# Optimization experiments

Measured on AMD Instinct MI355X. Metric: run time of the kernel, lower is better.

## Reference

```python
import jax, jax.numpy as jnp
import numpy as np

NB = 2        # trm_num_blocks
H = 4         # trm_num_heads
D = 128       # trm_hidden_dim
L = 512
B = 1
PAD = 0
NEG = jnp.float32(-2**32 + 1)


def _ln(x, g, b, eps=1e-8):
    m = x.mean(-1, keepdims=True)
    v = x.var(-1, keepdims=True)
    return (x - m) / jnp.sqrt(v + eps) * g + b


def setup_inputs() -> dict:
    key = jax.random.key(0)
    ks = jax.random.split(key, 16)
    s = 0.02
    inp = {
        "log_seqs": jax.random.randint(ks[0], (B, L), 0, 1000),
        "seqs": jax.random.normal(ks[1], (B, L, D), jnp.float32),
        "time_matrix_K": jax.random.normal(ks[2], (B, L, L, D), jnp.float32),
        # per-block stacked params [NB, ...]
        "Wq": jax.random.normal(ks[3], (NB, D, D), jnp.float32) * s,
        "bq": jnp.zeros((NB, D), jnp.float32),
        "Wk": jax.random.normal(ks[4], (NB, D, D), jnp.float32) * s,
        "bk": jnp.zeros((NB, D), jnp.float32),
        "Wv": jax.random.normal(ks[5], (NB, D, D), jnp.float32) * s,
        "bv": jnp.zeros((NB, D), jnp.float32),
        "Wt": jax.random.normal(ks[6], (NB, D, D), jnp.float32) * s,
        "bt": jnp.zeros((NB, D), jnp.float32),
        "Wtp": jax.random.normal(ks[7], (NB, D, 1), jnp.float32) * s,
        "btp": jnp.zeros((NB, 1), jnp.float32),
        "ln1_g": jnp.ones((NB, D), jnp.float32),
        "ln1_b": jnp.zeros((NB, D), jnp.float32),
        "ln2_g": jnp.ones((NB, D), jnp.float32),
        "ln2_b": jnp.zeros((NB, D), jnp.float32),
        "W1": jax.random.normal(ks[8], (NB, D, D), jnp.float32) * s,
        "b1": jnp.zeros((NB, D), jnp.float32),
        "W2": jax.random.normal(ks[9], (NB, D, D), jnp.float32) * s,
        "b2": jnp.zeros((NB, D), jnp.float32),
        "lnf_g": jnp.ones((D,), jnp.float32),
        "lnf_b": jnp.zeros((D,), jnp.float32),
    }
    return inp


def reference(log_seqs, seqs, time_matrix_K, Wq, bq, Wk, bk, Wv, bv, Wt, bt,
              Wtp, btp, ln1_g, ln1_b, ln2_g, ln2_b, W1, b1, W2, b2, lnf_g, lnf_b):
    hd = D // H
    pad = (log_seqs == PAD)                     # [B, L] True at padding
    keep = (~pad)[..., None].astype(seqs.dtype)  # [B, L, 1]
    seqs = seqs * keep
    causal = ~jnp.tril(jnp.ones((L, L), bool))  # True above diagonal (masked)
    # combined mask [1, B, L, L]: pad query rows OR non-causal entries
    mask = pad[None, :, :, None] | causal[None, None, :, :]

    attn_ws = []
    for i in range(NB):
        Q = _ln(seqs, ln1_g[i], ln1_b[i])
        q = Q @ Wq[i] + bq[i]
        k = seqs @ Wk[i] + bk[i]
        v = seqs @ Wv[i] + bv[i]
        # head-major layout [H, B, L, hd] (matches torch split+cat along dim 0)
        qh = q.reshape(B, L, H, hd).transpose(2, 0, 1, 3)
        kh = k.reshape(B, L, H, hd).transpose(2, 0, 1, 3)
        vh = v.reshape(B, L, H, hd).transpose(2, 0, 1, 3)
        scores = jnp.einsum('hbqd,hbkd->hbqk', qh, kh)  # [H, B, L, L]
        # time bias: sigmoid(proj(relu(W_t t))) in (0,1); log is negative
        tw = jax.nn.sigmoid(
            (jax.nn.relu(time_matrix_K @ Wt[i] + bt[i]) @ Wtp[i] + btp[i]).squeeze(-1)
        )                                             # [B, L, L]
        scores = (scores + jnp.log(tw)) / jnp.float32(hd) ** 0.5
        scores = jnp.where(mask, NEG, scores)
        w = jax.nn.softmax(scores, axis=-1)           # dropout is identity (eval)
        attn_ws.append(w.reshape(H * B, L, L))
        out = jnp.einsum('hbqk,hbkd->hbqd', w, vh).transpose(1, 2, 0, 3).reshape(B, L, D)
        seqs = Q + out
        x = _ln(seqs, ln2_g[i], ln2_b[i])
        y = jax.nn.relu(x @ W1[i] + b1[i]) @ W2[i] + b2[i]
        seqs = (x + y) * keep                         # FFN residual adds post-LN x
    log_feats = _ln(seqs, lnf_g, lnf_b)
    return (log_feats, tuple(attn_ws))
```

## Files before the change

### kernel.cpp

```cpp
#include <hip/hip_runtime.h>

#define L 512
#define D 128
#define H 4
#define HD 32

typedef __bf16 bf16x8 __attribute__((ext_vector_type(8)));
typedef float  f32x4  __attribute__((ext_vector_type(4)));

__device__ __forceinline__ float wave_sum(float v){
#pragma unroll
  for (int o = 32; o; o >>= 1) v += __shfl_xor(v, o);
  return v;
}
__device__ __forceinline__ float wave_max(float v){
#pragma unroll
  for (int o = 32; o; o >>= 1) v = fmaxf(v, __shfl_xor(v, o));
  return v;
}

__global__ void k_bfrag(const float* __restrict__ Wt, unsigned short* __restrict__ bf){
  int idx = blockIdx.x * 256 + threadIdx.x;
  int jj   = idx & 7;
  int lane = (idx >> 3) & 63;
  int k0   = (idx >> 9) & 3;
  int nt   = idx >> 11;
  int d    = k0 * 32 + (lane >> 4) * 8 + jj;
  int col  = (nt & 7) * 16 + (lane & 15);
  int blk  = nt >> 3;
  float v = Wt[blk * D * D + d * D + col];
  __bf16 h = (__bf16)v;
  unsigned short us;
  __builtin_memcpy(&us, &h, 2);
  bf[idx] = us;
}

__global__ __launch_bounds__(256, 2) void k_timebias(
    const float* __restrict__ T, const unsigned short* __restrict__ bfg,
    const float* __restrict__ bt, const float* __restrict__ wtp,
    const float* __restrict__ btp, float* __restrict__ logtw){
  __shared__ __align__(16) unsigned short bsh[32768];
  __shared__ float bts[256], wtps[256];
  int tid = threadIdx.x;
  {
    const uint4* g = (const uint4*)bfg;
    uint4* s = (uint4*)bsh;
#pragma unroll
    for (int i = 0; i < 16; ++i) s[tid + i * 256] = g[tid + i * 256];
    bts[tid]  = bt[tid];
    wtps[tid] = wtp[tid];
  }
  __syncthreads();

  int lane = tid & 63, w = tid >> 6;
  int quad = lane >> 4, m = lane & 15;
  const bf16x8* bls = (const bf16x8*)bsh;
  int wbase = blockIdx.x * 256 + w * 64;

  bf16x8 afr[4][4];
#pragma unroll
  for (int mt = 0; mt < 4; ++mt){
    const float* tp = T + (size_t)(wbase + mt * 16 + m) * D + quad * 8;
#pragma unroll
    for (int k0 = 0; k0 < 4; ++k0){
      float4 f0 = *(const float4*)(tp + k0 * 32);
      float4 f1 = *(const float4*)(tp + k0 * 32 + 4);
      bf16x8 a;
      a[0] = (__bf16)f0.x; a[1] = (__bf16)f0.y; a[2] = (__bf16)f0.z; a[3] = (__bf16)f0.w;
      a[4] = (__bf16)f1.x; a[5] = (__bf16)f1.y; a[6] = (__bf16)f1.z; a[7] = (__bf16)f1.w;
      afr[mt][k0] = a;
    }
  }

#pragma unroll
  for (int blk = 0; blk < 2; ++blk){
    f32x4 rs[4] = {{0,0,0,0},{0,0,0,0},{0,0,0,0},{0,0,0,0}};
#pragma unroll
    for (int ntl = 0; ntl < 8; ++ntl){
      int nt = blk * 8 + ntl;
      f32x4 acc[4] = {{0,0,0,0},{0,0,0,0},{0,0,0,0},{0,0,0,0}};
#pragma unroll
      for (int k0 = 0; k0 < 4; ++k0){
        bf16x8 b = bls[(nt * 4 + k0) * 64 + lane];
#pragma unroll
        for (int mt = 0; mt < 4; ++mt)
          acc[mt] = __builtin_amdgcn_mfma_f32_16x16x32_bf16(afr[mt][k0], b, acc[mt], 0, 0, 0);
      }
      float btv = bts[nt * 16 + m];
      float wtv = wtps[nt * 16 + m];
#pragma unroll
      for (int mt = 0; mt < 4; ++mt)
#pragma unroll
        for (int r = 0; r < 4; ++r)
          rs[mt][r] += fmaxf(acc[mt][r] + btv, 0.f) * wtv;
    }
#pragma unroll
    for (int mt = 0; mt < 4; ++mt)
#pragma unroll
      for (int r = 0; r < 4; ++r){
        float v = rs[mt][r];
        v += __shfl_xor(v, 1); v += __shfl_xor(v, 2);
        v += __shfl_xor(v, 4); v += __shfl_xor(v, 8);
        rs[mt][r] = v;
      }
    if (m == 0){
      float bp = btp[blk];
      float* out = logtw + blk * (L * L);
#pragma unroll
      for (int mt = 0; mt < 4; ++mt){
        float4 o;
        float s0 = rs[mt][0] + bp; o.x = -logf(1.f + expf(-s0));
        float s1 = rs[mt][1] + bp; o.y = -logf(1.f + expf(-s1));
        float s2 = rs[mt][2] + bp; o.z = -logf(1.f + expf(-s2));
        float s3 = rs[mt][3] + bp; o.w = -logf(1.f + expf(-s3));
        *(float4*)(out + wbase + mt * 16 + quad * 4) = o;
      }
    }
  }
}

__global__ __launch_bounds__(128) void k_qkv(
    const float* __restrict__ src, const int* __restrict__ ls, int domask,
    const float* __restrict__ g1, const float* __restrict__ b1,
    const float* __restrict__ Wq, const float* __restrict__ bq,
    const float* __restrict__ Wk, const float* __restrict__ bk,
    const float* __restrict__ Wv, const float* __restrict__ bv,
    float* __restrict__ Q, float* __restrict__ qo,
    float* __restrict__ kT, float* __restrict__ vo){
  __shared__ float xs[128], Qs[128], tmp[2];
  int row = blockIdx.x, c = threadIdx.x;
  float xv = src[row * D + c];
  if (domask && ls[row] == 0) xv = 0.f;
  float s = wave_sum(xv);
  if ((c & 63) == 0) tmp[c >> 6] = s;
  __syncthreads();
  float mean = (tmp[0] + tmp[1]) * (1.f / 128.f);
  __syncthreads();
  float dv = xv - mean;
  float s2 = wave_sum(dv * dv);
  if ((c & 63) == 0) tmp[c >> 6] = s2;
  __syncthreads();
  float var = fmaxf((tmp[0] + tmp[1]) * (1.f / 128.f), 0.f);
  float qn = dv * rsqrtf(var + 1e-8f) * g1[c] + b1[c];
  xs[c] = xv; Qs[c] = qn;
  Q[row * D + c] = qn;
  __syncthreads();
  float aq = 0.f, ak = 0.f, av = 0.f;
#pragma unroll 4
  for (int k = 0; k < 128; ++k){
    float xq = Qs[k], xk = xs[k];
    aq += xq * Wq[k * D + c];
    ak += xk * Wk[k * D + c];
    av += xk * Wv[k * D + c];
  }
  aq += bq[c]; ak += bk[c]; av += bv[c];
  qo[row * D + c] = aq;
  vo[row * D + c] = av;
  kT[(c >> 5) * (HD * L) + (c & 31) * L + row] = ak;
}

__global__ __launch_bounds__(256) void k_attn_ffn(
    const float* __restrict__ qb, const float* __restrict__ kT, const float* __restrict__ vb,
    const float* __restrict__ logtw, const int* __restrict__ ls,
    const float* __restrict__ Q,
    const float* __restrict__ g2, const float* __restrict__ b2,
    const float* __restrict__ W1, const float* __restrict__ b1f,
    const float* __restrict__ W2, const float* __restrict__ b2f,
    const float* __restrict__ lg, const float* __restrict__ lb,
    float* __restrict__ wout, float* __restrict__ xout,
    float* __restrict__ lf, int last){
  __shared__ float qsh[128];
  __shared__ float sc[4][512];
  __shared__ float xr[128];
  __shared__ float x2s[128];
  __shared__ float y1s[128];
  __shared__ float pstore[256];
  __shared__ float st[2];
  int qr = blockIdx.x;
  int tid = threadIdx.x;
  int lane = tid & 63, h = tid >> 6;

  if (tid < 128) qsh[tid] = qb[qr * D + tid];
  __syncthreads();

  const float* kh = kT + h * (HD * L);
  const float* ltw = logtw + qr * L;
  const float RS = 0.17677669529663687f;
  float s[8];
#pragma unroll
  for (int jj = 0; jj < 8; ++jj){
    int j = jj * 64 + lane;
    float d = 0.f;
#pragma unroll
    for (int dd = 0; dd < 32; ++dd) d += qsh[h * HD + dd] * kh[dd * L + j];
    s[jj] = (d + ltw[j]) * RS;
  }
  bool padq = (ls[qr] == 0);
  float wgt[8];
  if (padq){
#pragma unroll
    for (int jj = 0; jj < 8; ++jj) wgt[jj] = 1.f / 512.f;
  } else {
    float mx = -3e38f;
#pragma unroll
    for (int jj = 0; jj < 8; ++jj){ int j = jj * 64 + lane; if (j <= qr) mx = fmaxf(mx, s[jj]); }
    mx = wave_max(mx);
    float sum = 0.f;
#pragma unroll
    for (int jj = 0; jj < 8; ++jj){
      int j = jj * 64 + lane;
      float e = (j <= qr) ? expf(s[jj] - mx) : 0.f;
      wgt[jj] = e; sum += e;
    }
    sum = wave_sum(sum);
    float inv = 1.f / sum;
#pragma unroll
    for (int jj = 0; jj < 8; ++jj) wgt[jj] *= inv;
  }
  float* wrow = wout + h * (L * L) + qr * L;
#pragma unroll
  for (int jj = 0; jj < 8; ++jj){
    int j = jj * 64 + lane;
    sc[h][j] = wgt[jj];
    wrow[j] = wgt[jj];
  }
  __syncthreads();

  int g = lane >> 5, d2 = lane & 31;
  const float* vh = vb + h * HD + d2;
  const float* sch = sc[h];
  float acc = 0.f;
  for (int j = g * 256; j < g * 256 + 256; ++j) acc += sch[j] * vh[(size_t)j * D];
  acc += __shfl_xor(acc, 32);
  if (g == 0){
    int idx = qr * D + h * HD + d2;
    xr[h * HD + d2] = Q[idx] + acc;
  }
  __syncthreads();

  if (tid < 64){
    float a = xr[tid], b = xr[tid + 64];
    float s1 = wave_sum(a + b);
    float s2 = wave_sum(a * a + b * b);
    if (tid == 0){
      float mean = s1 * (1.f / 128.f);
      float var = fmaxf(s2 * (1.f / 128.f) - mean * mean, 0.f);
      st[0] = mean; st[1] = rsqrtf(var + 1e-8f);
    }
  }
  __syncthreads();
  int c = tid & 127, half = tid >> 7;
  if (half == 0) x2s[c] = (xr[c] - st[0]) * st[1] * g2[c] + b2[c];
  __syncthreads();

  float a1 = 0.f;
  {
    int k0 = half * 64;
#pragma unroll 8
    for (int k = 0; k < 64; ++k) a1 += x2s[k0 + k] * W1[(k0 + k) * D + c];
  }
  pstore[tid] = a1;
  __syncthreads();
  if (half == 0) y1s[c] = fmaxf(pstore[c] + pstore[c + 128] + b1f[c], 0.f);
  __syncthreads();

  float a2 = 0.f;
  {
    int k0 = half * 64;
#pragma unroll 8
    for (int k = 0; k < 64; ++k) a2 += y1s[k0 + k] * W2[(k0 + k) * D + c];
  }
  pstore[tid] = a2;
  __syncthreads();
  float kp = (ls[qr] != 0) ? 1.f : 0.f;
  if (half == 0){
    float xo = (x2s[c] + pstore[c] + pstore[c + 128] + b2f[c]) * kp;
    xr[c] = xo;
    if (!last) xout[qr * D + c] = xo;
  }
  __syncthreads();

  if (last){
    if (tid < 64){
      float a = xr[tid], b = xr[tid + 64];
      float s1 = wave_sum(a + b);
      float s2 = wave_sum(a * a + b * b);
      if (tid == 0){
        float mean = s1 * (1.f / 128.f);
        float var = fmaxf(s2 * (1.f / 128.f) - mean * mean, 0.f);
        st[0] = mean; st[1] = rsqrtf(var + 1e-8f);
      }
    }
    __syncthreads();
    if (half == 0) lf[qr * D + c] = (xr[c] - st[0]) * st[1] * lg[c] + lb[c];
  }
}

extern "C" void kernel_launch(void* const* d_in, const int* in_sizes, int n_in,
                              void* d_out, int out_size, void* d_ws, size_t ws_size,
                              hipStream_t stream){
  const int*   ls   = (const int*)d_in[0];
  const float* seqs = (const float*)d_in[1];
  const float* T    = (const float*)d_in[2];
  const float* Wq   = (const float*)d_in[3];
  const float* bq   = (const float*)d_in[4];
  const float* Wk   = (const float*)d_in[5];
  const float* bk   = (const float*)d_in[6];
  const float* Wv   = (const float*)d_in[7];
  const float* bv   = (const float*)d_in[8];
  const float* Wt   = (const float*)d_in[9];
  const float* bt   = (const float*)d_in[10];
  const float* Wtp  = (const float*)d_in[11];
  const float* btp  = (const float*)d_in[12];
  const float* g1   = (const float*)d_in[13];
  const float* b1   = (const float*)d_in[14];
  const float* g2   = (const float*)d_in[15];
  const float* b2   = (const float*)d_in[16];
  const float* W1   = (const float*)d_in[17];
  const float* b1f  = (const float*)d_in[18];
  const float* W2   = (const float*)d_in[19];
  const float* b2f  = (const float*)d_in[20];
  const float* lg   = (const float*)d_in[21];
  const float* lb   = (const float*)d_in[22];

  float* ws   = (float*)d_ws;
  float* x    = ws;
  float* Q    = x + 65536;
  float* qb   = Q + 65536;
  float* vb   = qb + 65536;
  float* kT   = vb + 65536;
  float* logtw= kT + 65536;
  unsigned short* bfg = (unsigned short*)(logtw + 2 * 262144);

  float* outF = (float*)d_out;
  float* lf = outF;
  float* w0 = outF + 65536;
  float* w1 = w0 + 1048576;

  k_bfrag   <<<128, 256, 0, stream>>>(Wt, bfg);
  k_timebias<<<1024, 256, 0, stream>>>(T, bfg, bt, Wtp, btp, logtw);

  for (int blk = 0; blk < 2; ++blk){
    int o = blk * D * D, ob = blk * D;
    const float* src = blk ? x : seqs;
    k_qkv <<<512, 128, 0, stream>>>(src, ls, blk == 0 ? 1 : 0,
                                    g1 + ob, b1 + ob, Wq + o, bq + ob,
                                    Wk + o, bk + ob, Wv + o, bv + ob,
                                    Q, qb, kT, vb);
    k_attn_ffn<<<512, 256, 0, stream>>>(qb, kT, vb, logtw + blk * (L * L), ls,
                                        Q, g2 + ob, b2 + ob, W1 + o, b1f + ob,
                                        W2 + o, b2f + ob, lg, lb,
                                        blk ? w1 : w0, x, lf, blk);
  }
}
```

Baseline: 327.3 us.

## Use bf16 MFMA for attention and fuse next block's QKV into FFN kernel

Attention is rewritten to handle a 16-query tile per head per workgroup. QK^T and PV run on bf16 MFMA instructions, with Q, K and V stored in pre-swizzled bf16 fragment layouts and the softmax reduced across waves through shared memory. The FFN is split into its own kernel, and that kernel also computes LN1 plus the QKV projection for the next block, or the final LayerNorm. The aim is to replace scalar fp32 dot products with matrix-core work and to cut a launch and round trips. The cost is bf16 rounding of Q, K, V and the probabilities, which may affect accuracy, plus more launches for the attention/FFN split.

```diff
diff --git a/kernel.cpp b/kernel.cpp
--- a/kernel.cpp
+++ b/kernel.cpp
@@ -13,10 +13,11 @@
   for (int o = 32; o; o >>= 1) v += __shfl_xor(v, o);
   return v;
 }
-__device__ __forceinline__ float wave_max(float v){
-#pragma unroll
-  for (int o = 32; o; o >>= 1) v = fmaxf(v, __shfl_xor(v, o));
-  return v;
+__device__ __forceinline__ unsigned short bfbits(float v){
+  __bf16 h = (__bf16)v;
+  unsigned short u;
+  __builtin_memcpy(&u, &h, 2);
+  return u;
 }
 
 __global__ void k_bfrag(const float* __restrict__ Wt, unsigned short* __restrict__ bf){
@@ -28,11 +29,7 @@
   int d    = k0 * 32 + (lane >> 4) * 8 + jj;
   int col  = (nt & 7) * 16 + (lane & 15);
   int blk  = nt >> 3;
-  float v = Wt[blk * D * D + d * D + col];
-  __bf16 h = (__bf16)v;
-  unsigned short us;
-  __builtin_memcpy(&us, &h, 2);
-  bf[idx] = us;
+  bf[idx] = bfbits(Wt[blk * D * D + d * D + col]);
 }
 
 __global__ __launch_bounds__(256, 2) void k_timebias(
@@ -119,18 +116,35 @@
   }
 }
 
-__global__ __launch_bounds__(128) void k_qkv(
-    const float* __restrict__ src, const int* __restrict__ ls, int domask,
+__device__ __forceinline__ void write_qA(unsigned short* qA, int row, int c, float v){
+  int qt = row >> 4, m = row & 15;
+  int h = c >> 5, cc = c & 31;
+  qA[(((qt * 4 + h) * 64) + (cc >> 3) * 16 + m) * 8 + (cc & 7)] = bfbits(v);
+}
+__device__ __forceinline__ void write_kB(unsigned short* kB, int row, int c, float v){
+  int h = c >> 5, cc = c & 31;
+  int nt = row >> 4;
+  kB[((h * 32 + nt) * 64 + (cc >> 3) * 16 + (row & 15)) * 8 + (cc & 7)] = bfbits(v);
+}
+__device__ __forceinline__ void write_vB(unsigned short* vB, int row, int c, float v){
+  int h = c >> 5, cc = c & 31;
+  int kk = row >> 5, qv = (row >> 3) & 3, jv = row & 7;
+  int nt = cc >> 4;
+  vB[(((h * 16 + kk) * 2 + nt) * 64 + qv * 16 + (cc & 15)) * 8 + jv] = bfbits(v);
+}
+
+__global__ __launch_bounds__(128) void k_qkv0(
+    const float* __restrict__ src, const int* __restrict__ ls,
     const float* __restrict__ g1, const float* __restrict__ b1,
     const float* __restrict__ Wq, const float* __restrict__ bq,
     const float* __restrict__ Wk, const float* __restrict__ bk,
     const float* __restrict__ Wv, const float* __restrict__ bv,
-    float* __restrict__ Q, float* __restrict__ qo,
-    float* __restrict__ kT, float* __restrict__ vo){
+    float* __restrict__ Q, unsigned short* __restrict__ qA,
+    unsigned short* __restrict__ kB, unsigned short* __restrict__ vB){
   __shared__ float xs[128], Qs[128], tmp[2];
   int row = blockIdx.x, c = threadIdx.x;
   float xv = src[row * D + c];
-  if (domask && ls[row] == 0) xv = 0.f;
+  if (ls[row] == 0) xv = 0.f;
   float s = wave_sum(xv);
   if ((c & 63) == 0) tmp[c >> 6] = s;
   __syncthreads();
@@ -153,93 +167,157 @@
     ak += xk * Wk[k * D + c];
     av += xk * Wv[k * D + c];
   }
-  aq += bq[c]; ak += bk[c]; av += bv[c];
-  qo[row * D + c] = aq;
-  vo[row * D + c] = av;
-  kT[(c >> 5) * (HD * L) + (c & 31) * L + row] = ak;
-}
-
-__global__ __launch_bounds__(256) void k_attn_ffn(
-    const float* __restrict__ qb, const float* __restrict__ kT, const float* __restrict__ vb,
-    const float* __restrict__ logtw, const int* __restrict__ ls,
-    const float* __restrict__ Q,
+  write_qA(qA, row, c, aq + bq[c]);
+  write_kB(kB, row, c, ak + bk[c]);
+  write_vB(vB, row, c, av + bv[c]);
+}
+
+__global__ __launch_bounds__(256) void k_attn(
+    const unsigned short* __restrict__ qA, const unsigned short* __restrict__ kB,
+    const unsigned short* __restrict__ vB, const float* __restrict__ logtw,
+    const int* __restrict__ ls, const float* __restrict__ Q,
+    float* __restrict__ wout, float* __restrict__ xr){
+  __shared__ __align__(16) unsigned short pa[16 * 64 * 8];
+  __shared__ float pvp[4][2][64][4];
+  __shared__ float smax[4][16], ssum[4][16];
+  int qt = blockIdx.x >> 2, h = blockIdx.x & 3;
+  int tid = threadIdx.x, lane = tid & 63, w = tid >> 6;
+  int quad = lane >> 4, mcol = lane & 15;
+  const float RS = 0.17677669529663687f;
+
+  bf16x8 qf = ((const bf16x8*)qA)[(qt * 4 + h) * 64 + lane];
+
+  f32x4 acc[8];
+#pragma unroll
+  for (int nt8 = 0; nt8 < 8; ++nt8){
+    bf16x8 bf = ((const bf16x8*)kB)[(h * 32 + w * 8 + nt8) * 64 + lane];
+    f32x4 z = {0, 0, 0, 0};
+    acc[nt8] = __builtin_amdgcn_mfma_f32_16x16x32_bf16(qf, bf, z, 0, 0, 0);
+  }
+
+  float e[8][4];
+  float mx4[4] = {-3e38f, -3e38f, -3e38f, -3e38f};
+#pragma unroll
+  for (int nt8 = 0; nt8 < 8; ++nt8){
+    int col = w * 128 + nt8 * 16 + mcol;
+#pragma unroll
+    for (int r = 0; r < 4; ++r){
+      int row = qt * 16 + quad * 4 + r;
+      float sv = (acc[nt8][r] + logtw[row * L + col]) * RS;
+      sv = (col <= row) ? sv : -3e38f;
+      e[nt8][r] = sv;
+      mx4[r] = fmaxf(mx4[r], sv);
+    }
+  }
+#pragma unroll
+  for (int r = 0; r < 4; ++r){
+    float v = mx4[r];
+    v = fmaxf(v, __shfl_xor(v, 1)); v = fmaxf(v, __shfl_xor(v, 2));
+    v = fmaxf(v, __shfl_xor(v, 4)); v = fmaxf(v, __shfl_xor(v, 8));
+    mx4[r] = v;
+  }
+  if (mcol == 0){
+#pragma unroll
+    for (int r = 0; r < 4; ++r) smax[w][quad * 4 + r] = mx4[r];
+  }
+  __syncthreads();
+  float mxr[4], sum4[4] = {0, 0, 0, 0};
+#pragma unroll
+  for (int r = 0; r < 4; ++r){
+    int rr = quad * 4 + r;
+    mxr[r] = fmaxf(fmaxf(smax[0][rr], smax[1][rr]), fmaxf(smax[2][rr], smax[3][rr]));
+  }
+#pragma unroll
+  for (int nt8 = 0; nt8 < 8; ++nt8)
+#pragma unroll
+    for (int r = 0; r < 4; ++r){
+      float sv = e[nt8][r];
+      float ev = (sv > -1e38f) ? expf(sv - mxr[r]) : 0.f;
+      e[nt8][r] = ev;
+      sum4[r] += ev;
+    }
+#pragma unroll
+  for (int r = 0; r < 4; ++r){
+    float v = sum4[r];
+    v += __shfl_xor(v, 1); v += __shfl_xor(v, 2);
+    v += __shfl_xor(v, 4); v += __shfl_xor(v, 8);
+    sum4[r] = v;
+  }
+  if (mcol == 0){
+#pragma unroll
+    for (int r = 0; r < 4; ++r) ssum[w][quad * 4 + r] = sum4[r];
+  }
+  __syncthreads();
+  float inv[4]; int padr[4];
+#pragma unroll
+  for (int r = 0; r < 4; ++r){
+    int rr = quad * 4 + r;
+    inv[r] = 1.f / (ssum[0][rr] + ssum[1][rr] + ssum[2][rr] + ssum[3][rr]);
+    padr[r] = (ls[qt * 16 + rr] == 0);
+  }
+#pragma unroll
+  for (int nt8 = 0; nt8 < 8; ++nt8){
+    int col = w * 128 + nt8 * 16 + mcol;
+    int kk = col >> 5, qk = (col >> 3) & 3, jj = col & 7;
+#pragma unroll
+    for (int r = 0; r < 4; ++r){
+      int rl = quad * 4 + r;
+      float wv = padr[r] ? (1.f / 512.f) : e[nt8][r] * inv[r];
+      wout[h * (L * L) + (qt * 16 + rl) * L + col] = wv;
+      pa[(kk * 64 + qk * 16 + rl) * 8 + jj] = bfbits(wv);
+    }
+  }
+
+  f32x4 pacc[2] = {{0,0,0,0},{0,0,0,0}};
+#pragma unroll
+  for (int kk4 = 0; kk4 < 4; ++kk4){
+    int kk = w * 4 + kk4;
+    bf16x8 af = ((const bf16x8*)pa)[kk * 64 + lane];
+#pragma unroll
+    for (int nt = 0; nt < 2; ++nt){
+      bf16x8 bf = ((const bf16x8*)vB)[((h * 16 + kk) * 2 + nt) * 64 + lane];
+      pacc[nt] = __builtin_amdgcn_mfma_f32_16x16x32_bf16(af, bf, pacc[nt], 0, 0, 0);
+    }
+  }
+#pragma unroll
+  for (int nt = 0; nt < 2; ++nt)
+#pragma unroll
+    for (int r = 0; r < 4; ++r) pvp[w][nt][lane][r] = pacc[nt][r];
+  __syncthreads();
+  if (w < 2){
+    int nt = w;
+#pragma unroll
+    for (int r = 0; r < 4; ++r){
+      float o = pvp[0][nt][lane][r] + pvp[1][nt][lane][r]
+              + pvp[2][nt][lane][r] + pvp[3][nt][lane][r];
+      int row = qt * 16 + quad * 4 + r;
+      int cg = h * HD + nt * 16 + mcol;
+      xr[row * D + cg] = Q[row * D + cg] + o;
+    }
+  }
+}
+
+__global__ __launch_bounds__(256) void k_ffn(
+    const float* __restrict__ xr, const int* __restrict__ ls,
     const float* __restrict__ g2, const float* __restrict__ b2,
     const float* __restrict__ W1, const float* __restrict__ b1f,
     const float* __restrict__ W2, const float* __restrict__ b2f,
-    const float* __restrict__ lg, const float* __restrict__ lb,
-    float* __restrict__ wout, float* __restrict__ xout,
-    float* __restrict__ lf, int last){
-  __shared__ float qsh[128];
-  __shared__ float sc[4][512];
-  __shared__ float xr[128];
-  __shared__ float x2s[128];
-  __shared__ float y1s[128];
-  __shared__ float pstore[256];
-  __shared__ float st[2];
-  int qr = blockIdx.x;
-  int tid = threadIdx.x;
-  int lane = tid & 63, h = tid >> 6;
-
-  if (tid < 128) qsh[tid] = qb[qr * D + tid];
-  __syncthreads();
-
-  const float* kh = kT + h * (HD * L);
-  const float* ltw = logtw + qr * L;
-  const float RS = 0.17677669529663687f;
-  float s[8];
-#pragma unroll
-  for (int jj = 0; jj < 8; ++jj){
-    int j = jj * 64 + lane;
-    float d = 0.f;
-#pragma unroll
-    for (int dd = 0; dd < 32; ++dd) d += qsh[h * HD + dd] * kh[dd * L + j];
-    s[jj] = (d + ltw[j]) * RS;
-  }
-  bool padq = (ls[qr] == 0);
-  float wgt[8];
-  if (padq){
-#pragma unroll
-    for (int jj = 0; jj < 8; ++jj) wgt[jj] = 1.f / 512.f;
-  } else {
-    float mx = -3e38f;
-#pragma unroll
-    for (int jj = 0; jj < 8; ++jj){ int j = jj * 64 + lane; if (j <= qr) mx = fmaxf(mx, s[jj]); }
-    mx = wave_max(mx);
-    float sum = 0.f;
-#pragma unroll
-    for (int jj = 0; jj < 8; ++jj){
-      int j = jj * 64 + lane;
-      float e = (j <= qr) ? expf(s[jj] - mx) : 0.f;
-      wgt[jj] = e; sum += e;
-    }
-    sum = wave_sum(sum);
-    float inv = 1.f / sum;
-#pragma unroll
-    for (int jj = 0; jj < 8; ++jj) wgt[jj] *= inv;
-  }
-  float* wrow = wout + h * (L * L) + qr * L;
-#pragma unroll
-  for (int jj = 0; jj < 8; ++jj){
-    int j = jj * 64 + lane;
-    sc[h][j] = wgt[jj];
-    wrow[j] = wgt[jj];
-  }
-  __syncthreads();
-
-  int g = lane >> 5, d2 = lane & 31;
-  const float* vh = vb + h * HD + d2;
-  const float* sch = sc[h];
-  float acc = 0.f;
-  for (int j = g * 256; j < g * 256 + 256; ++j) acc += sch[j] * vh[(size_t)j * D];
-  acc += __shfl_xor(acc, 32);
-  if (g == 0){
-    int idx = qr * D + h * HD + d2;
-    xr[h * HD + d2] = Q[idx] + acc;
-  }
-  __syncthreads();
-
+    int fuse_qkv,
+    const float* __restrict__ g1, const float* __restrict__ b1,
+    const float* __restrict__ Wq, const float* __restrict__ bq,
+    const float* __restrict__ Wk, const float* __restrict__ bk,
+    const float* __restrict__ Wv, const float* __restrict__ bv,
+    float* __restrict__ Q, unsigned short* __restrict__ qA,
+    unsigned short* __restrict__ kB, unsigned short* __restrict__ vB,
+    int fuse_lnf, const float* __restrict__ lg, const float* __restrict__ lb,
+    float* __restrict__ lf){
+  __shared__ float xrs[128], x2s[128], y1s[128], pstore[256], st[2];
+  int row = blockIdx.x, tid = threadIdx.x;
+  int c = tid & 127, half = tid >> 7;
+  if (half == 0) xrs[c] = xr[row * D + c];
+  __syncthreads();
   if (tid < 64){
-    float a = xr[tid], b = xr[tid + 64];
+    float a = xrs[tid], b = xrs[tid + 64];
     float s1 = wave_sum(a + b);
     float s2 = wave_sum(a * a + b * b);
     if (tid == 0){
@@ -249,40 +327,30 @@
     }
   }
   __syncthreads();
-  int c = tid & 127, half = tid >> 7;
-  if (half == 0) x2s[c] = (xr[c] - st[0]) * st[1] * g2[c] + b2[c];
-  __syncthreads();
-
+  if (half == 0) x2s[c] = (xrs[c] - st[0]) * st[1] * g2[c] + b2[c];
+  __syncthreads();
   float a1 = 0.f;
-  {
-    int k0 = half * 64;
+  { int k0 = half * 64;
 #pragma unroll 8
-    for (int k = 0; k < 64; ++k) a1 += x2s[k0 + k] * W1[(k0 + k) * D + c];
-  }
+    for (int k = 0; k < 64; ++k) a1 += x2s[k0 + k] * W1[(k0 + k) * D + c]; }
   pstore[tid] = a1;
   __syncthreads();
   if (half == 0) y1s[c] = fmaxf(pstore[c] + pstore[c + 128] + b1f[c], 0.f);
   __syncthreads();
-
   float a2 = 0.f;
-  {
-    int k0 = half * 64;
+  { int k0 = half * 64;
 #pragma unroll 8
-    for (int k = 0; k < 64; ++k) a2 += y1s[k0 + k] * W2[(k0 + k) * D + c];
-  }
+    for (int k = 0; k < 64; ++k) a2 += y1s[k0 + k] * W2[(k0 + k) * D + c]; }
   pstore[tid] = a2;
   __syncthreads();
-  float kp = (ls[qr] != 0) ? 1.f : 0.f;
-  if (half == 0){
-    float xo = (x2s[c] + pstore[c] + pstore[c + 128] + b2f[c]) * kp;
-    xr[c] = xo;
-    if (!last) xout[qr * D + c] = xo;
-  }
-  __syncthreads();
-
-  if (last){
+  float kp = (ls[row] != 0) ? 1.f : 0.f;
+  if (half == 0)
+    xrs[c] = (x2s[c] + pstore[c] + pstore[c + 128] + b2f[c]) * kp;
+  __syncthreads();
+
+  if (fuse_qkv){
     if (tid < 64){
-      float a = xr[tid], b = xr[tid + 64];
+      float a = xrs[tid], b = xrs[tid + 64];
       float s1 = wave_sum(a + b);
       float s2 = wave_sum(a * a + b * b);
       if (tid == 0){
@@ -292,7 +360,47 @@
       }
     }
     __syncthreads();
-    if (half == 0) lf[qr * D + c] = (xr[c] - st[0]) * st[1] * lg[c] + lb[c];
+    if (half == 0){
+      float qn = (xrs[c] - st[0]) * st[1] * g1[c] + b1[c];
+      y1s[c] = qn;
+      Q[row * D + c] = qn;
+    }
+    __syncthreads();
+    float avp = 0.f;
+    if (half == 0){
+      float aq = 0.f;
+#pragma unroll 4
+      for (int k = 0; k < 128; ++k) aq += y1s[k] * Wq[k * D + c];
+#pragma unroll 8
+      for (int k = 0; k < 64; ++k) avp += xrs[k] * Wv[k * D + c];
+      write_qA(qA, row, c, aq + bq[c]);
+    } else {
+      float ak = 0.f;
+#pragma unroll 4
+      for (int k = 0; k < 128; ++k) ak += xrs[k] * Wk[k * D + c];
+#pragma unroll 8
+      for (int k = 64; k < 128; ++k) avp += xrs[k] * Wv[k * D + c];
+      write_kB(kB, row, c, ak + bk[c]);
+    }
+    pstore[tid] = avp;
+    __syncthreads();
+    if (half == 1)
+      write_vB(vB, row, c, pstore[c] + pstore[c + 128] + bv[c]);
+  }
+
+  if (fuse_lnf){
+    if (tid < 64){
+      float a = xrs[tid], b = xrs[tid + 64];
+      float s1 = wave_sum(a + b);
+      float s2 = wave_sum(a * a + b * b);
+      if (tid == 0){
+        float mean = s1 * (1.f / 128.f);
+        float var = fmaxf(s2 * (1.f / 128.f) - mean * mean, 0.f);
+        st[0] = mean; st[1] = rsqrtf(var + 1e-8f);
+      }
+    }
+    __syncthreads();
+    if (half == 0) lf[row * D + c] = (xrs[c] - st[0]) * st[1] * lg[c] + lb[c];
   }
 }
 
@@ -323,14 +431,14 @@
   const float* lg   = (const float*)d_in[21];
   const float* lb   = (const float*)d_in[22];
 
-  float* ws   = (float*)d_ws;
-  float* x    = ws;
-  float* Q    = x + 65536;
-  float* qb   = Q + 65536;
-  float* vb   = qb + 65536;
-  float* kT   = vb + 65536;
-  float* logtw= kT + 65536;
+  float* ws    = (float*)d_ws;
+  float* Q     = ws;
+  float* xr    = Q + 65536;
+  float* logtw = xr + 65536;
   unsigned short* bfg = (unsigned short*)(logtw + 2 * 262144);
+  unsigned short* qA  = bfg + 32768;
+  unsigned short* kB  = qA + 65536;
+  unsigned short* vB  = kB + 65536;
 
   float* outF = (float*)d_out;
   float* lf = outF;
@@ -340,16 +448,18 @@
   k_bfrag   <<<128, 256, 0, stream>>>(Wt, bfg);
   k_timebias<<<1024, 256, 0, stream>>>(T, bfg, bt, Wtp, btp, logtw);
 
-  for (int blk = 0; blk < 2; ++blk){
-    int o = blk * D * D, ob = blk * D;
-    const float* src = blk ? x : seqs;
-    k_qkv <<<512, 128, 0, stream>>>(src, ls, blk == 0 ? 1 : 0,
-                                    g1 + ob, b1 + ob, Wq + o, bq + ob,
-                                    Wk + o, bk + ob, Wv + o, bv + ob,
-                                    Q, qb, kT, vb);
-    k_attn_ffn<<<512, 256, 0, stream>>>(qb, kT, vb, logtw + blk * (L * L), ls,
-                                        Q, g2 + ob, b2 + ob, W1 + o, b1f + ob,
-                                        W2 + o, b2f + ob, lg, lb,
-                                        blk ? w1 : w0, x, lf, blk);
-  }
-}
+  k_qkv0<<<512, 128, 0, stream>>>(seqs, ls, g1, b1, Wq, bq, Wk, bk, Wv, bv,
+                                  Q, qA, kB, vB);
+  k_attn<<<128, 256, 0, stream>>>(qA, kB, vB, logtw, ls, Q, w0, xr);
+  k_ffn<<<512, 256, 0, stream>>>(xr, ls, g2, b2, W1, b1f, W2, b2f,
+                                 1, g1 + D, b1 + D, Wq + D * D, bq + D,
+                                 Wk + D * D, bk + D, Wv + D * D, bv + D,
+                                 Q, qA, kB, vB,
+                                 0, lg, lb, lf);
+  k_attn<<<128, 256, 0, stream>>>(qA, kB, vB, logtw + L * L, ls, Q, w1, xr);
+  k_ffn<<<512, 256, 0, stream>>>(xr, ls, g2 + D, b2 + D, W1 + D * D, b1f + D,
+                                 W2 + D * D, b2f + D,
+                                 0, g1, b1, Wq, bq, Wk, bk, Wv, bv,
+                                 Q, qA, kB, vB,
+                                 1, lg, lb, lf);
+}
```

After: 321.0 us. No clear change (-1.9%).
